# Kernel tuning notes

Hardware: AMD Instinct MI355X
Metric: run time of the kernel (lower is better)

Reference implementation:

```python
import math
import jax, jax.numpy as jnp
import numpy as np

# Matryoshka nested sizes (num_heads == 1, kv_groups == 1)
QK_SIZES = [512, 1024, 1536, 2048]
HEAD_SIZES = [512, 1024, 1536, 2048]
D_IN = 2048   # input_sizes[-1]
D_OUT = 2048  # output_sizes[-1]
NEG = -1e9


def setup_inputs() -> dict:
    key = jax.random.key(0)
    ks = jax.random.split(key, 5)
    B, S = 4, 2048
    x = jax.random.normal(ks[0], (B, S, D_IN), dtype=jnp.float32)
    mask = jnp.tril(jnp.ones((S, S), dtype=bool))  # causal boolean mask
    scale = 0.02
    Wq = jax.random.normal(ks[1], (D_IN, QK_SIZES[-1]), dtype=jnp.float32) * scale
    Wk = jax.random.normal(ks[2], (D_IN, QK_SIZES[-1]), dtype=jnp.float32) * scale
    Wv = jax.random.normal(ks[3], (D_IN, HEAD_SIZES[-1]), dtype=jnp.float32) * scale
    Wo = jax.random.normal(ks[4], (HEAD_SIZES[-1], D_OUT), dtype=jnp.float32) * scale
    return {"x": x, "mask": mask, "Wq": Wq, "Wk": Wk, "Wv": Wv, "Wo": Wo}


def reference(x, mask, Wq, Wk, Wv, Wo):
    # x: [B, S, D_IN]; num_heads == 1 so we keep heads implicit.
    q = x @ Wq  # [B, S, qk_last]
    k = x @ Wk  # [B, S, qk_last]
    v = x @ Wv  # [B, S, head_last]
    mask_add = jnp.where(mask, 0.0, NEG).astype(x.dtype)  # [S, S]

    outs = []
    cum = None  # cumulative QK^T across nested qk slices
    prev_qk = 0
    prev_h = 0
    for qk, h in zip(QK_SIZES, HEAD_SIZES):
        dp = jnp.einsum("bqd,bkd->bqk", q[..., prev_qk:qk], k[..., prev_qk:qk])
        cum = dp if cum is None else cum + dp  # [B, S, S]
        logits = cum * (1.0 / math.sqrt(qk)) + mask_add
        attn = jax.nn.softmax(logits, axis=-1)
        outs.append(jnp.einsum("bqk,bkd->bqd", attn, v[..., prev_h:h]))
        prev_qk, prev_h = qk, h
    o = jnp.concatenate(outs, axis=-1)  # [B, S, head_last]
    return o @ Wo  # [B, S, D_OUT]
```

## Files before the change

kernel.cpp:

```cpp
#include <hip/hip_runtime.h>


typedef __attribute__((ext_vector_type(8))) short bf16x8;
typedef __attribute__((ext_vector_type(4))) float f32x4;
typedef unsigned short u16;
typedef unsigned int u32;

__device__ __forceinline__ u16 f2bf(float f) {
  union { float f; u32 u; } v; v.f = f;
  u32 r = v.u + 0x7fffu + ((v.u >> 16) & 1u);
  return (u16)(r >> 16);
}
__device__ __forceinline__ float bf2f(u16 b) {
  union { u32 u; float f; } v; v.u = ((u32)b) << 16;
  return v.f;
}
struct alignas(16) U16x8 { u16 v[8]; };

#define GLDS(gp, lp)                                                      \
  __builtin_amdgcn_global_load_lds(                                       \
      (const __attribute__((address_space(1))) void*)(gp),                \
      (__attribute__((address_space(3))) void*)(lp), 16, 0, 0)


__global__ __launch_bounds__(256) void conv_f32_bf16(const float* __restrict__ in,
                                                     u16* __restrict__ out) {
  size_t i = ((size_t)blockIdx.x * 256 + threadIdx.x) * 8;
  float4 a = *(const float4*)(in + i);
  float4 b = *(const float4*)(in + i + 4);
  U16x8 w;
  w.v[0] = f2bf(a.x); w.v[1] = f2bf(a.y); w.v[2] = f2bf(a.z); w.v[3] = f2bf(a.w);
  w.v[4] = f2bf(b.x); w.v[5] = f2bf(b.y); w.v[6] = f2bf(b.z); w.v[7] = f2bf(b.w);
  *(U16x8*)(out + i) = w;
}

__global__ __launch_bounds__(256) void transpose_conv4(const float* __restrict__ W0,
                                                       const float* __restrict__ W1,
                                                       const float* __restrict__ W2,
                                                       const float* __restrict__ W3,
                                                       u16* __restrict__ out) {
  const int D = 2048;
  const float* in = (blockIdx.z == 0) ? W0 : (blockIdx.z == 1) ? W1
                  : (blockIdx.z == 2) ? W2 : W3;
  u16* o = out + (size_t)blockIdx.z * D * D;
  __shared__ float t[32][33];
  int bx = blockIdx.x * 32, by = blockIdx.y * 32;
  int tx = threadIdx.x & 31, ty = threadIdx.x >> 5;
#pragma unroll
  for (int i = 0; i < 32; i += 8)
    t[ty + i][tx] = in[(size_t)(by + ty + i) * D + bx + tx];
  __syncthreads();
#pragma unroll
  for (int i = 0; i < 32; i += 8)
    o[(size_t)(bx + ty + i) * D + by + tx] = f2bf(t[tx][ty + i]);
}

__global__ __launch_bounds__(256) void transpose_bf16(const u16* __restrict__ in,
                                                      u16* __restrict__ out) {
  const int D = 2048;
  size_t zoff = (size_t)blockIdx.z * D * D;
  in += zoff; out += zoff;
  __shared__ u16 t[32][34];
  int bx = blockIdx.x * 32, by = blockIdx.y * 32;
  int tx = threadIdx.x & 31, ty = threadIdx.x >> 5;
#pragma unroll
  for (int i = 0; i < 32; i += 8)
    t[ty + i][tx] = in[(size_t)(by + ty + i) * D + bx + tx];
  __syncthreads();
#pragma unroll
  for (int i = 0; i < 32; i += 8)
    out[(size_t)(bx + ty + i) * D + by + tx] = t[tx][ty + i];
}

template <bool OUT_BF16>
__global__ __launch_bounds__(512, 2) void gemmQKV(
    const u16* __restrict__ A, int lda,
    const u16* __restrict__ B, int ldb,
    void* __restrict__ Cv, int ldc,
    int K, int nmat, long long sBm, long long sCm) {
  extern __shared__ char smem[];
  u16* const As = (u16*)smem;
  u16* const Bs = (u16*)(smem + 65536);

  const u32 wg = blockIdx.x;
  const int n0 = (int)(wg & 7u) * 256;
  const u32 c = wg >> 3;
  const int mat = (int)(c % (u32)nmat);
  const int m0 = (int)(c / (u32)nmat) * 256;

  B += (size_t)mat * sBm;

  const int tid = threadIdx.x;
  const int lane = tid & 63, wave = tid >> 6;
  const int wm = (wave >> 2) * 128;
  const int wn = (wave & 3) * 64;
  const int fr = lane & 15, kgrp = lane >> 4;
  const u32 lo = (u32)(wave * 1024);

  const int srow = tid >> 2;
  const int ssl = (tid & 3) ^ ((srow >> 1) & 3);
  const u16* gA0 = A + (size_t)(m0 + srow) * lda + ssl * 8;
  const u16* gA1 = gA0 + (size_t)128 * lda;
  const u16* gB0 = B + (size_t)(n0 + srow) * ldb + ssl * 8;
  const u16* gB1 = gB0 + (size_t)128 * ldb;

  const int koe = (kgrp ^ ((fr >> 1) & 3)) * 8;

#define STG(slot, kOff) do {                                              \
    char* la = (char*)As + (slot) * 16384 + lo;                           \
    char* lb = (char*)Bs + (slot) * 16384 + lo;                           \
    GLDS(gA0 + (kOff), la);                                               \
    GLDS(gA1 + (kOff), la + 8192);                                        \
    GLDS(gB0 + (kOff), lb);                                               \
    GLDS(gB1 + (kOff), lb + 8192);                                        \
  } while (0)

#define READF(FA, FB, sl) do {                                            \
    const u16* as_ = As + (sl) * 8192;                                    \
    const u16* bs_ = Bs + (sl) * 8192;                                    \
    _Pragma("unroll") for (int n_ = 0; n_ < 4; ++n_)                      \
      FB[n_] = *(const bf16x8*)&bs_[((wn + n_ * 16 + fr) << 5) + koe];    \
    _Pragma("unroll") for (int m_ = 0; m_ < 8; ++m_)                      \
      FA[m_] = *(const bf16x8*)&as_[((wm + m_ * 16 + fr) << 5) + koe];    \
  } while (0)

#define MMCL(FA, FB) do {                                                 \
    __builtin_amdgcn_s_setprio(1);                                        \
    _Pragma("unroll") for (int m_ = 0; m_ < 8; ++m_)                      \
    _Pragma("unroll") for (int n_ = 0; n_ < 4; ++n_)                      \
      acc[m_][n_] = __builtin_amdgcn_mfma_f32_16x16x32_bf16(              \
          FA[m_], FB[n_], acc[m_][n_], 0, 0, 0);                          \
    __builtin_amdgcn_s_setprio(0);                                        \
  } while (0)

#define ITER(tt, CA, CB, NA, NB) do {                                     \
    if ((tt) + 3 < NT)                                                    \
      asm volatile("s_waitcnt lgkmcnt(12)" ::: "memory");                 \
    if ((tt) <= NT - 3)                                                   \
      asm volatile("s_waitcnt vmcnt(4)" ::: "memory");                    \
    else if ((tt) == NT - 2)                                              \
      asm volatile("s_waitcnt vmcnt(0)" ::: "memory");                    \
    if ((tt) <= NT - 2) {                                                 \
      __builtin_amdgcn_s_barrier();                                       \
      __builtin_amdgcn_sched_barrier(0);                                  \
    }                                                                     \
    if ((tt) + 3 < NT) STG(((tt) + 3) & 3, ((tt) + 3) * 32);              \
    if ((tt) + 1 < NT) READF(NA, NB, ((tt) + 1) & 3);                     \
    MMCL(CA, CB);                                                         \
  } while (0)

  f32x4 acc[8][4];
#pragma unroll
  for (int m = 0; m < 8; ++m)
#pragma unroll
    for (int n = 0; n < 4; ++n)
#pragma unroll
      for (int j = 0; j < 4; ++j) acc[m][n][j] = 0.f;

  const int NT = K >> 5;
  bf16x8 fA0[8], fB0[4], fA1[8], fB1[4];

  STG(0, 0);
  STG(1, 32);
  STG(2, 64);
  asm volatile("s_waitcnt vmcnt(8)" ::: "memory");
  __builtin_amdgcn_s_barrier();
  __builtin_amdgcn_sched_barrier(0);
  READF(fA0, fB0, 0);

  for (int tt = 0; tt < NT; tt += 2) {
    ITER(tt, fA0, fB0, fA1, fB1);
    ITER(tt + 1, fA1, fB1, fA0, fB0);
  }
#undef ITER
#undef MMCL
#undef READF
#undef STG

  const int cl = lane & 15, rb = (lane >> 4) * 4;
  if (OUT_BF16) {
    u16* C = (u16*)Cv + (size_t)mat * sCm;
#pragma unroll
    for (int m = 0; m < 8; ++m)
#pragma unroll
      for (int n = 0; n < 4; ++n)
#pragma unroll
        for (int j = 0; j < 4; ++j)
          C[(size_t)(m0 + wm + m * 16 + rb + j) * ldc + (n0 + wn + n * 16 + cl)] =
              f2bf(acc[m][n][j]);
  } else {
    float* C = (float*)Cv + (size_t)mat * sCm;
#pragma unroll
    for (int m = 0; m < 8; ++m)
#pragma unroll
      for (int n = 0; n < 4; ++n)
#pragma unroll
        for (int j = 0; j < 4; ++j)
          C[(size_t)(m0 + wm + m * 16 + rb + j) * ldc + (n0 + wn + n * 16 + cl)] =
              acc[m][n][j];
  }
}

template <bool OUT_BF16>
__global__ __launch_bounds__(256, 2) void gemm128(
    const u16* __restrict__ A, int lda,
    const u16* __restrict__ B, int ldb,
    void* __restrict__ Cv, int ldc,
    int K, int nmat, long long sBm, long long sCm) {
  constexpr int RPS = 64;
  extern __shared__ char smem[];
  u16* const As = (u16*)smem;
  u16* const Bs = (u16*)smem + 2 * 128 * 32;

  const u32 wg = blockIdx.x;
  const int n0 = (int)(wg & 7u) * 256;
  const u32 c = wg >> 3;
  const int mat = (int)(c % (u32)nmat);
  const int m0 = (int)(c / (u32)nmat) * 128;

  B += (size_t)mat * sBm;

  const int tid = threadIdx.x;
  const int lane = tid & 63, wave = tid >> 6;
  const int wn = (wave & 3) * 64;
  const int fr = lane & 15, kgrp = lane >> 4;
  const u32 lo = (u32)(wave * 1024);

  const int srow = tid >> 2;
  const int ssl = (tid & 3) ^ ((srow >> 1) & 3);
  const u16* gA = A + (size_t)(m0 + srow) * lda + ssl * 8;
  const u16* gB = B + (size_t)(n0 + srow) * ldb + ssl * 8;

  const int koe = (kgrp ^ ((fr >> 1) & 3)) * 8;

#define STG(slot, kOff) do {                                              \
    char* la = (char*)As + (slot) * 8192 + lo;                            \
    char* lb = (char*)Bs + (slot) * 16384 + lo;                           \
    _Pragma("unroll") for (int j_ = 0; j_ < 2; ++j_)                      \
      GLDS(gA + (size_t)j_ * RPS * lda + (kOff), la + j_ * RPS * 64);     \
    _Pragma("unroll") for (int j_ = 0; j_ < 4; ++j_)                      \
      GLDS(gB + (size_t)j_ * RPS * ldb + (kOff), lb + j_ * RPS * 64);     \
  } while (0)

#define READF(FA, FB, sl) do {                                            \
    const u16* as_ = As + (sl) * 4096;                                    \
    const u16* bs_ = Bs + (sl) * 8192;                                    \
    _Pragma("unroll") for (int n_ = 0; n_ < 4; ++n_)                      \
      FB[n_] = *(const bf16x8*)&bs_[((wn + n_ * 16 + fr) << 5) + koe];    \
    _Pragma("unroll") for (int m_ = 0; m_ < 8; ++m_)                      \
      FA[m_] = *(const bf16x8*)&as_[(((m_ * 16 + fr)) << 5) + koe];       \
  } while (0)

#define MMCL(FA, FB) do {                                                 \
    __builtin_amdgcn_s_setprio(1);                                        \
    _Pragma("unroll") for (int m_ = 0; m_ < 8; ++m_)                      \
    _Pragma("unroll") for (int n_ = 0; n_ < 4; ++n_)                      \
      acc[m_][n_] = __builtin_amdgcn_mfma_f32_16x16x32_bf16(              \
          FA[m_], FB[n_], acc[m_][n_], 0, 0, 0);                          \
    __builtin_amdgcn_s_setprio(0);                                        \
  } while (0)

#define ITER(tt, CA, CB, NA, NB) do {                                     \
    if ((tt) + 1 < NT) READF(NA, NB, ((tt) + 1) & 1);                     \
    if ((tt) + 2 < NT) {                                                  \
      asm volatile("s_waitcnt lgkmcnt(12)" ::: "memory");                 \
      __builtin_amdgcn_s_barrier();                                       \
      STG((tt) & 1, ((tt) + 2) * 32);                                     \
      __builtin_amdgcn_sched_barrier(0);                                  \
    }                                                                     \
    MMCL(CA, CB);                                                         \
    if ((tt) + 2 < NT) {                                                  \
      asm volatile("s_waitcnt vmcnt(0)" ::: "memory");                    \
      __builtin_amdgcn_s_barrier();                                       \
    }                                                                     \
  } while (0)

  f32x4 acc[8][4];
#pragma unroll
  for (int m = 0; m < 8; ++m)
#pragma unroll
    for (int n = 0; n < 4; ++n)
#pragma unroll
      for (int j = 0; j < 4; ++j) acc[m][n][j] = 0.f;

  const int NT = K >> 5;
  bf16x8 fA0[8], fB0[4], fA1[8], fB1[4];

  STG(0, 0);
  STG(1, 32);
  asm volatile("s_waitcnt vmcnt(0)" ::: "memory");
  __builtin_amdgcn_s_barrier();
  __builtin_amdgcn_sched_barrier(0);
  READF(fA0, fB0, 0);

  for (int tt = 0; tt < NT; tt += 2) {
    ITER(tt, fA0, fB0, fA1, fB1);
    ITER(tt + 1, fA1, fB1, fA0, fB0);
  }
#undef ITER
#undef MMCL
#undef READF
#undef STG

  const int cl = lane & 15, rb = (lane >> 4) * 4;
  if (OUT_BF16) {
    u16* C = (u16*)Cv + (size_t)mat * sCm;
#pragma unroll
    for (int m = 0; m < 8; ++m)
#pragma unroll
      for (int n = 0; n < 4; ++n)
#pragma unroll
        for (int j = 0; j < 4; ++j)
          C[(size_t)(m0 + m * 16 + rb + j) * ldc + (n0 + wn + n * 16 + cl)] =
              f2bf(acc[m][n][j]);
  } else {
    float* C = (float*)Cv + (size_t)mat * sCm;
#pragma unroll
    for (int m = 0; m < 8; ++m)
#pragma unroll
      for (int n = 0; n < 4; ++n)
#pragma unroll
        for (int j = 0; j < 4; ++j)
          C[(size_t)(m0 + m * 16 + rb + j) * ldc + (n0 + wn + n * 16 + cl)] =
              acc[m][n][j];
  }
}

__global__ __launch_bounds__(256) void qk_mega(
    const u16* __restrict__ A, const u16* __restrict__ B,
    u16* __restrict__ snapA, u16* __restrict__ snapB,
    float scaleA, float scaleB,
    const u16* __restrict__ initSrc, float initScale) {
  const int lda = 2048;
  const int m0 = blockIdx.y * 128, n0 = blockIdx.x * 128;
  if (n0 >= m0 + 128) return;
  const size_t zWE = (size_t)blockIdx.z * 4194304ull;
  extern __shared__ char smem[];
  u16* const As = (u16*)smem;
  u16* const Bs = (u16*)(smem + 32768);

  const int tid = threadIdx.x;
  const int lane = tid & 63, wave = tid >> 6;
  const int wm = (wave >> 1) * 64, wn = (wave & 1) * 64;
  const int fr = lane & 15;
  const int col = lane & 15, rb = (lane >> 4) * 4;
  const u32 lo = (u32)(wave * 1024);

  const int srow = tid >> 2;
  const int ssl = (tid & 3) ^ ((srow >> 1) & 3);
  const u16* gA0 = A + zWE + (size_t)(m0 + srow) * lda + ssl * 8;
  const u16* gA1 = gA0 + (size_t)64 * lda;
  const u16* gB0 = B + zWE + (size_t)(n0 + srow) * lda + ssl * 8;
  const u16* gB1 = gB0 + (size_t)64 * lda;

  const int koe = ((lane >> 4) ^ ((fr >> 1) & 3)) * 8;

#define QSTG(slot, kOff) do {                                             \
    char* la = (char*)As + (slot) * 8192 + lo;                            \
    char* lb = (char*)Bs + (slot) * 8192 + lo;                            \
    GLDS(gA0 + (kOff), la);                                               \
    GLDS(gA1 + (kOff), la + 4096);                                        \
    GLDS(gB0 + (kOff), lb);                                               \
    GLDS(gB1 + (kOff), lb + 4096);                                        \
  } while (0)

#define QREADF(FA, FB, sl) do {                                           \
    const u16* as_ = As + (sl) * 4096;                                    \
    const u16* bs_ = Bs + (sl) * 4096;                                    \
    _Pragma("unroll") for (int n_ = 0; n_ < 4; ++n_)                      \
      FB[n_] = *(const bf16x8*)&bs_[((wn + n_ * 16 + fr) << 5) + koe];    \
    _Pragma("unroll") for (int m_ = 0; m_ < 4; ++m_)                      \
      FA[m_] = *(const bf16x8*)&as_[((wm + m_ * 16 + fr) << 5) + koe];    \
  } while (0)

#define QMMCL(FA, FB) do {                                                \
    __builtin_amdgcn_s_setprio(1);                                        \
    _Pragma("unroll") for (int m_ = 0; m_ < 4; ++m_)                      \
    _Pragma("unroll") for (int n_ = 0; n_ < 4; ++n_)                      \
      acc[m_][n_] = __builtin_amdgcn_mfma_f32_16x16x32_bf16(              \
          FA[m_], FB[n_], acc[m_][n_], 0, 0, 0);                          \
    __builtin_amdgcn_s_setprio(0);                                        \
  } while (0)

#define QITER(tt, CA, CB, NA, NB) do {                                    \
    if ((tt) + 3 < 32)                                                    \
      asm volatile("s_waitcnt lgkmcnt(8)" ::: "memory");                  \
    if ((tt) <= 29)                                                       \
      asm volatile("s_waitcnt vmcnt(4)" ::: "memory");                    \
    else if ((tt) == 30)                                                  \
      asm volatile("s_waitcnt vmcnt(0)" ::: "memory");                    \
    if ((tt) <= 30) {                                                     \
      __builtin_amdgcn_s_barrier();                                       \
      __builtin_amdgcn_sched_barrier(0);                                  \
    }                                                                     \
    if ((tt) + 3 < 32) QSTG(((tt) + 3) & 3, ((tt) + 3) * 32);             \
    if ((tt) + 1 < 32) QREADF(NA, NB, ((tt) + 1) & 3);                    \
    QMMCL(CA, CB);                                                        \
  } while (0)

  f32x4 acc[4][4];
  if (initSrc) {
    const u16* ip = initSrc + zWE;
#pragma unroll
    for (int m = 0; m < 4; ++m)
#pragma unroll
      for (int n = 0; n < 4; ++n)
#pragma unroll
        for (int j = 0; j < 4; ++j)
          acc[m][n][j] = bf2f(ip[(size_t)(m0 + wm + m * 16 + rb + j) * 2048 +
                                 (n0 + wn + n * 16 + col)]) * initScale;
  } else {
#pragma unroll
    for (int m = 0; m < 4; ++m)
#pragma unroll
      for (int n = 0; n < 4; ++n)
#pragma unroll
        for (int j = 0; j < 4; ++j) acc[m][n][j] = 0.f;
  }

#define SNAPW(ptr, scl)                                                                \
  do {                                                                                 \
    u16* sp = (ptr) + zWE;                                                             \
    _Pragma("unroll") for (int m = 0; m < 4; ++m)                                      \
    _Pragma("unroll") for (int n = 0; n < 4; ++n)                                      \
    _Pragma("unroll") for (int j = 0; j < 4; ++j)                                      \
        sp[(size_t)(m0 + wm + m * 16 + rb + j) * 2048 + (n0 + wn + n * 16 + col)] =    \
            f2bf(acc[m][n][j] * (scl));                                                \
  } while (0)

  bf16x8 fA0[4], fB0[4], fA1[4], fB1[4];
  QSTG(0, 0);
  QSTG(1, 32);
  QSTG(2, 64);
  asm volatile("s_waitcnt vmcnt(8)" ::: "memory");
  __builtin_amdgcn_s_barrier();
  __builtin_amdgcn_sched_barrier(0);
  QREADF(fA0, fB0, 0);

  for (int tt = 0; tt < 32; tt += 2) {
    QITER(tt, fA0, fB0, fA1, fB1);
    QITER(tt + 1, fA1, fB1, fA0, fB0);
    if (tt == 14) SNAPW(snapA, scaleA);
  }
  SNAPW(snapB, scaleB);
#undef QITER
#undef QMMCL
#undef QREADF
#undef QSTG
#undef SNAPW
}

__global__ __launch_bounds__(256) void gemm_pv(
    const u16* __restrict__ A0, const u16* __restrict__ A1,
    const u16* __restrict__ vT, u16* __restrict__ o, int s0) {
  const int z = blockIdx.z;
  const int half = z >> 2, b = z & 3, s = s0 + half;
  const u16* A = (half ? A1 : A0) + (size_t)b * 4194304ull;
  const u16* B = vT + (size_t)b * 4194304ull + (size_t)s * 512 * 2048;
  u16* C = o + (size_t)b * 4194304ull + s * 512;

  const int n0 = blockIdx.x * 128, m0 = blockIdx.y * 128;
  const int NT = (m0 + 128) >> 5;
  extern __shared__ char smem[];
  u16* const As = (u16*)smem;
  u16* const Bs = (u16*)(smem + 32768);

  const int tid = threadIdx.x;
  const int lane = tid & 63, wave = tid >> 6;
  const int wm = (wave >> 1) * 64, wn = (wave & 1) * 64;
  const int fr = lane & 15;
  const u32 lo = (u32)(wave * 1024);

  const int srow = tid >> 2;
  const int ssl = (tid & 3) ^ ((srow >> 1) & 3);
  const u16* gA0 = A + (size_t)(m0 + srow) * 2048 + ssl * 8;
  const u16* gA1 = gA0 + (size_t)64 * 2048;
  const u16* gB0 = B + (size_t)(n0 + srow) * 2048 + ssl * 8;
  const u16* gB1 = gB0 + (size_t)64 * 2048;

  const int koe = ((lane >> 4) ^ ((fr >> 1) & 3)) * 8;

#define PSTG(slot, kOff) do {                                             \
    char* la = (char*)As + (slot) * 8192 + lo;                            \
    char* lb = (char*)Bs + (slot) * 8192 + lo;                            \
    GLDS(gA0 + (kOff), la);                                               \
    GLDS(gA1 + (kOff), la + 4096);                                        \
    GLDS(gB0 + (kOff), lb);                                               \
    GLDS(gB1 + (kOff), lb + 4096);                                        \
  } while (0)

#define PREADF(FA, FB, sl) do {                                           \
    const u16* as_ = As + (sl) * 4096;                                    \
    const u16* bs_ = Bs + (sl) * 4096;                                    \
    _Pragma("unroll") for (int n_ = 0; n_ < 4; ++n_)                      \
      FB[n_] = *(const bf16x8*)&bs_[((wn + n_ * 16 + fr) << 5) + koe];    \
    _Pragma("unroll") for (int m_ = 0; m_ < 4; ++m_)                      \
      FA[m_] = *(const bf16x8*)&as_[((wm + m_ * 16 + fr) << 5) + koe];    \
  } while (0)

#define PMMCL(FA, FB) do {                                                \
    __builtin_amdgcn_s_setprio(1);                                        \
    _Pragma("unroll") for (int m_ = 0; m_ < 4; ++m_)                      \
    _Pragma("unroll") for (int n_ = 0; n_ < 4; ++n_)                      \
      acc[m_][n_] = __builtin_amdgcn_mfma_f32_16x16x32_bf16(              \
          FA[m_], FB[n_], acc[m_][n_], 0, 0, 0);                          \
    __builtin_amdgcn_s_setprio(0);                                        \
  } while (0)

#define PITER(tt, CA, CB, NA, NB) do {                                    \
    if ((tt) + 3 < NT)                                                    \
      asm volatile("s_waitcnt lgkmcnt(8)" ::: "memory");                  \
    if ((tt) <= NT - 3)                                                   \
      asm volatile("s_waitcnt vmcnt(4)" ::: "memory");                    \
    else if ((tt) == NT - 2)                                              \
      asm volatile("s_waitcnt vmcnt(0)" ::: "memory");                    \
    if ((tt) <= NT - 2) {                                                 \
      __builtin_amdgcn_s_barrier();                                       \
      __builtin_amdgcn_sched_barrier(0);                                  \
    }                                                                     \
    if ((tt) + 3 < NT) PSTG(((tt) + 3) & 3, ((tt) + 3) * 32);             \
    if ((tt) + 1 < NT) PREADF(NA, NB, ((tt) + 1) & 3);                    \
    PMMCL(CA, CB);                                                        \
  } while (0)

  f32x4 acc[4][4];
#pragma unroll
  for (int m = 0; m < 4; ++m)
#pragma unroll
    for (int n = 0; n < 4; ++n)
#pragma unroll
      for (int j = 0; j < 4; ++j) acc[m][n][j] = 0.f;

  bf16x8 fA0[4], fB0[4], fA1[4], fB1[4];
  PSTG(0, 0);
  PSTG(1, 32);
  PSTG(2, 64);
  asm volatile("s_waitcnt vmcnt(8)" ::: "memory");
  __builtin_amdgcn_s_barrier();
  __builtin_amdgcn_sched_barrier(0);
  PREADF(fA0, fB0, 0);

  for (int tt = 0; tt < NT; tt += 2) {
    PITER(tt, fA0, fB0, fA1, fB1);
    PITER(tt + 1, fA1, fB1, fA0, fB0);
  }
#undef PITER
#undef PMMCL
#undef PREADF
#undef PSTG

  const int col = lane & 15, rb = (lane >> 4) * 4;
#pragma unroll
  for (int m = 0; m < 4; ++m)
#pragma unroll
    for (int n = 0; n < 4; ++n)
#pragma unroll
      for (int j = 0; j < 4; ++j)
        C[(size_t)(m0 + wm + m * 16 + rb + j) * 2048 + (n0 + wn + n * 16 + col)] =
            f2bf(acc[m][n][j]);
}

__global__ __launch_bounds__(256) void softmax_dual(const u16* __restrict__ in0,
                                                    u16* __restrict__ out0,
                                                    const u16* __restrict__ in1,
                                                    u16* __restrict__ out1) {
  const int S = 2048;
  const int y = blockIdx.y;
  const u16* in  = (y < 4) ? in0  : in1;
  u16* out       = (y < 4) ? out0 : out1;
  const size_t WEz = (size_t)S * S * (y & 3);
  const int r = blockIdx.x;
  const int tid = threadIdx.x;
  const int lane = tid & 63, wave = tid >> 6;
  const int c0 = tid * 8;
  const int nvalid = r + 1;
  const int nwrite = (r & ~127) + 128;
  const u16* rowp = in + WEz + (size_t)r * S;

  float x[8];
  if (c0 < nvalid) {
    U16x8 a = *(const U16x8*)(rowp + c0);
#pragma unroll
    for (int i = 0; i < 8; ++i) x[i] = bf2f(a.v[i]);
  } else {
#pragma unroll
    for (int i = 0; i < 8; ++i) x[i] = 0.f;
  }

  float mx = -3e38f;
#pragma unroll
  for (int i = 0; i < 8; ++i)
    if (c0 + i < nvalid) mx = fmaxf(mx, x[i]);
#pragma unroll
  for (int off = 32; off > 0; off >>= 1) mx = fmaxf(mx, __shfl_xor(mx, off));
  __shared__ float redm[4], reds[4];
  if (lane == 0) redm[wave] = mx;
  __syncthreads();
  mx = fmaxf(fmaxf(redm[0], redm[1]), fmaxf(redm[2], redm[3]));

  float e[8], sum = 0.f;
#pragma unroll
  for (int i = 0; i < 8; ++i) {
    e[i] = (c0 + i < nvalid) ? __expf(x[i] - mx) : 0.f;
    sum += e[i];
  }
#pragma unroll
  for (int off = 32; off > 0; off >>= 1) sum += __shfl_xor(sum, off);
  if (lane == 0) reds[wave] = sum;
  __syncthreads();
  sum = reds[0] + reds[1] + reds[2] + reds[3];
  float inv = 1.f / sum;

  if (c0 < nwrite) {
    U16x8 w;
#pragma unroll
    for (int i = 0; i < 8; ++i) w.v[i] = f2bf(e[i] * inv);
    *(U16x8*)(out + WEz + (size_t)r * S + c0) = w;
  }
}

extern "C" void kernel_launch(void* const* d_in, const int* in_sizes, int n_in,
                              void* d_out, int out_size, void* d_ws, size_t ws_size,
                              hipStream_t stream) {
  (void)in_sizes; (void)n_in; (void)out_size; (void)ws_size;
  const float* x  = (const float*)d_in[0];
  const float* Wq = (const float*)d_in[2];
  const float* Wk = (const float*)d_in[3];
  const float* Wv = (const float*)d_in[4];
  const float* Wo = (const float*)d_in[5];
  float* out = (float*)d_out;

  char* w = (char*)d_ws;
  const size_t R  = 33554432ull;
  const long long WE = 4194304LL;

  u16* xb  = (u16*)(w);
  u16* wT  = (u16*)(w + R);
  u16* wqT = wT;
  u16* woT = wT + 3 * WE;
  u16* q   = (u16*)(w + 2 * R);
  u16* kk  = (u16*)(w + 3 * R);
  u16* v   = (u16*)(w + 4 * R);
  u16* vT  = (u16*)(w + 5 * R);
  u16* o   = v;
  u16* attnx = xb;
  u16* slot0 = (u16*)d_out;
  u16* slot1 = slot0 + 16777216ull;

  const float sc0 = 1.0f / sqrtf(512.0f);
  const float sc1 = 1.0f / sqrtf(1024.0f);
  const float sc2 = 1.0f / sqrtf(1536.0f);
  const float sc3 = 1.0f / sqrtf(2048.0f);

  hipFuncSetAttribute(reinterpret_cast<const void*>(&gemmQKV<true>),
                      hipFuncAttributeMaxDynamicSharedMemorySize, 131072);
  hipFuncSetAttribute(reinterpret_cast<const void*>(&gemm128<false>),
                      hipFuncAttributeMaxDynamicSharedMemorySize, 49152);
  hipFuncSetAttribute(reinterpret_cast<const void*>(&qk_mega),
                      hipFuncAttributeMaxDynamicSharedMemorySize, 65536);
  hipFuncSetAttribute(reinterpret_cast<const void*>(&gemm_pv),
                      hipFuncAttributeMaxDynamicSharedMemorySize, 65536);

  conv_f32_bf16<<<8192, 256, 0, stream>>>(x, xb);
  transpose_conv4<<<dim3(64, 64, 4), 256, 0, stream>>>(Wq, Wk, Wv, Wo, wT);
  gemmQKV<true><<<dim3(768), 512, 131072, stream>>>(
      xb, 2048, wqT, 2048, q, 2048, 2048, 3, WE, 16777216LL);
  transpose_bf16<<<dim3(64, 64, 4), 256, 0, stream>>>(v, vT);
  qk_mega<<<dim3(16, 16, 4), 256, 65536, stream>>>(q, kk, slot0, slot1, sc0, sc1,
                                                   nullptr, 0.f);
  softmax_dual<<<dim3(2048, 8), 256, 0, stream>>>(slot0, slot0, slot1, attnx);
  gemm_pv<<<dim3(4, 16, 8), 256, 65536, stream>>>(slot0, attnx, vT, o, 0);
  qk_mega<<<dim3(16, 16, 4), 256, 65536, stream>>>(q + 1024, kk + 1024, slot0,
                                                   slot1, sc2, sc3, slot1, 32.0f);
  softmax_dual<<<dim3(2048, 8), 256, 0, stream>>>(slot0, slot0, slot1, slot1);
  gemm_pv<<<dim3(4, 16, 8), 256, 65536, stream>>>(slot0, slot1, vT, o, 2);
  gemm128<false><<<dim3(512), 256, 49152, stream>>>(
      o, 2048, woT, 2048, out, 2048, 2048, 1, 0LL, 0LL);
}
```

Baseline: 529.6 us.

## Rewrite projection GEMM as eight-phase pipelined kernel and reuse it for output projection

Replaces the QKV GEMM main loop with an eight-phase schedule per 128-wide K chunk. Each phase loads half the A fragments and issues one half-tile global-to-LDS load, then runs a smaller MFMA cluster between barriers, with a changed LDS swizzle. The separate 128-row output-projection GEMM is removed and the same 256x256 kernel is used for it, launching 256 workgroups of 512 threads instead of 512 of 256. K is hardcoded to 2048, and the extra barriers plus fewer output-projection workgroups may reduce occupancy or overlap.

```diff
diff --git a/kernel.cpp b/kernel.cpp
--- a/kernel.cpp
+++ b/kernel.cpp
@@ -73,21 +73,19 @@
 }
 
 template <bool OUT_BF16>
-__global__ __launch_bounds__(512, 2) void gemmQKV(
+__global__ __launch_bounds__(512, 2) void gemm8p(
     const u16* __restrict__ A, int lda,
     const u16* __restrict__ B, int ldb,
     void* __restrict__ Cv, int ldc,
-    int K, int nmat, long long sBm, long long sCm) {
+    int nmat, long long sBm, long long sCm) {
   extern __shared__ char smem[];
-  u16* const As = (u16*)smem;
-  u16* const Bs = (u16*)(smem + 65536);
+  u16* const S = (u16*)smem;
 
   const u32 wg = blockIdx.x;
   const int n0 = (int)(wg & 7u) * 256;
   const u32 c = wg >> 3;
   const int mat = (int)(c % (u32)nmat);
   const int m0 = (int)(c / (u32)nmat) * 256;
-
   B += (size_t)mat * sBm;
 
   const int tid = threadIdx.x;
@@ -98,55 +96,45 @@
   const u32 lo = (u32)(wave * 1024);
 
   const int srow = tid >> 2;
-  const int ssl = (tid & 3) ^ ((srow >> 1) & 3);
-  const u16* gA0 = A + (size_t)(m0 + srow) * lda + ssl * 8;
-  const u16* gA1 = gA0 + (size_t)128 * lda;
-  const u16* gB0 = B + (size_t)(n0 + srow) * ldb + ssl * 8;
-  const u16* gB1 = gB0 + (size_t)128 * ldb;
-
-  const int koe = (kgrp ^ ((fr >> 1) & 3)) * 8;
-
-#define STG(slot, kOff) do {                                              \
-    char* la = (char*)As + (slot) * 16384 + lo;                           \
-    char* lb = (char*)Bs + (slot) * 16384 + lo;                           \
-    GLDS(gA0 + (kOff), la);                                               \
-    GLDS(gA1 + (kOff), la + 8192);                                        \
-    GLDS(gB0 + (kOff), lb);                                               \
-    GLDS(gB1 + (kOff), lb + 8192);                                        \
-  } while (0)
-
-#define READF(FA, FB, sl) do {                                            \
-    const u16* as_ = As + (sl) * 8192;                                    \
-    const u16* bs_ = Bs + (sl) * 8192;                                    \
-    _Pragma("unroll") for (int n_ = 0; n_ < 4; ++n_)                      \
-      FB[n_] = *(const bf16x8*)&bs_[((wn + n_ * 16 + fr) << 5) + koe];    \
-    _Pragma("unroll") for (int m_ = 0; m_ < 8; ++m_)                      \
-      FA[m_] = *(const bf16x8*)&as_[((wm + m_ * 16 + fr) << 5) + koe];    \
-  } while (0)
-
-#define MMCL(FA, FB) do {                                                 \
-    __builtin_amdgcn_s_setprio(1);                                        \
-    _Pragma("unroll") for (int m_ = 0; m_ < 8; ++m_)                      \
-    _Pragma("unroll") for (int n_ = 0; n_ < 4; ++n_)                      \
-      acc[m_][n_] = __builtin_amdgcn_mfma_f32_16x16x32_bf16(              \
-          FA[m_], FB[n_], acc[m_][n_], 0, 0, 0);                          \
-    __builtin_amdgcn_s_setprio(0);                                        \
-  } while (0)
-
-#define ITER(tt, CA, CB, NA, NB) do {                                     \
-    if ((tt) + 3 < NT)                                                    \
-      asm volatile("s_waitcnt lgkmcnt(12)" ::: "memory");                 \
-    if ((tt) <= NT - 3)                                                   \
-      asm volatile("s_waitcnt vmcnt(4)" ::: "memory");                    \
-    else if ((tt) == NT - 2)                                              \
-      asm volatile("s_waitcnt vmcnt(0)" ::: "memory");                    \
-    if ((tt) <= NT - 2) {                                                 \
-      __builtin_amdgcn_s_barrier();                                       \
-      __builtin_amdgcn_sched_barrier(0);                                  \
-    }                                                                     \
-    if ((tt) + 3 < NT) STG(((tt) + 3) & 3, ((tt) + 3) * 32);              \
-    if ((tt) + 1 < NT) READF(NA, NB, ((tt) + 1) & 3);                     \
-    MMCL(CA, CB);                                                         \
+  const int g = (tid & 3) ^ (srow & 3);
+  const u16* gA = A + (size_t)(m0 + srow) * lda + g * 8;
+  const u16* gB = B + (size_t)(n0 + srow) * ldb + g * 8;
+
+  const int rbase = (kgrp ^ (fr & 3)) * 8;
+  const int aoff = (wm + fr) * 32 + rbase;
+  const int boff = 32768 + (wn + fr) * 32 + rbase;
+
+#define STG8(ISB, slot, koff) do {                                       \
+    char* d_ = (char*)smem + ((ISB) ? 65536 : 0) + (slot) * 16384 + lo;  \
+    const u16* gp_ = (ISB) ? gB : gA;                                    \
+    const int ld_ = (ISB) ? ldb : lda;                                   \
+    GLDS(gp_ + (koff), d_);                                              \
+    GLDS(gp_ + (size_t)128 * ld_ + (koff), d_ + 8192);                   \
+  } while (0)
+
+#define PH8(LP, kb, DOSTG, WC) do {                                      \
+    constexpr int sl_ = (LP) >> 1;                                       \
+    constexpr int mh_ = (LP) & 1;                                        \
+    if (mh_ == 0) {                                                      \
+      _Pragma("unroll") for (int n_ = 0; n_ < 4; ++n_)                   \
+        fB[n_] = *(const bf16x8*)&S[boff + sl_ * 8192 + n_ * 512];       \
+    }                                                                    \
+    _Pragma("unroll") for (int a_ = 0; a_ < 4; ++a_)                     \
+      fA[a_] = *(const bf16x8*)&S[aoff + sl_ * 8192 + mh_ * 2048 + a_ * 512]; \
+    if (DOSTG) STG8(mh_, (3 + sl_) & 3, (kb) + (3 + sl_) * 32);          \
+    if ((WC) == 4) asm volatile("s_waitcnt vmcnt(4)" ::: "memory");      \
+    else if ((WC) == 0) asm volatile("s_waitcnt vmcnt(0)" ::: "memory"); \
+    __builtin_amdgcn_s_barrier();                                        \
+    asm volatile("s_waitcnt lgkmcnt(0)" ::: "memory");                   \
+    __builtin_amdgcn_sched_barrier(0);                                   \
+    __builtin_amdgcn_s_setprio(1);                                       \
+    _Pragma("unroll") for (int a_ = 0; a_ < 4; ++a_)                     \
+      _Pragma("unroll") for (int n_ = 0; n_ < 4; ++n_)                   \
+        acc[mh_ * 4 + a_][n_] = __builtin_amdgcn_mfma_f32_16x16x32_bf16( \
+            fA[a_], fB[n_], acc[mh_ * 4 + a_][n_], 0, 0, 0);             \
+    __builtin_amdgcn_s_setprio(0);                                       \
+    __builtin_amdgcn_s_barrier();                                        \
+    __builtin_amdgcn_sched_barrier(0);                                   \
   } while (0)
 
   f32x4 acc[8][4];
@@ -157,25 +145,31 @@
 #pragma unroll
       for (int j = 0; j < 4; ++j) acc[m][n][j] = 0.f;
 
-  const int NT = K >> 5;
-  bf16x8 fA0[8], fB0[4], fA1[8], fB1[4];
-
-  STG(0, 0);
-  STG(1, 32);
-  STG(2, 64);
+  bf16x8 fA[4], fB[4];
+
+  STG8(0, 0, 0);   STG8(1, 0, 0);
+  STG8(0, 1, 32);  STG8(1, 1, 32);
+  STG8(0, 2, 64);  STG8(1, 2, 64);
   asm volatile("s_waitcnt vmcnt(8)" ::: "memory");
   __builtin_amdgcn_s_barrier();
   __builtin_amdgcn_sched_barrier(0);
-  READF(fA0, fB0, 0);
-
-  for (int tt = 0; tt < NT; tt += 2) {
-    ITER(tt, fA0, fB0, fA1, fB1);
-    ITER(tt + 1, fA1, fB1, fA0, fB0);
-  }
-#undef ITER
-#undef MMCL
-#undef READF
-#undef STG
+
+  for (int i = 0; i < 15; ++i) {
+    const int kb = i * 128;
+    PH8(0, kb, 1, -1);  PH8(1, kb, 1, 4);
+    PH8(2, kb, 1, -1);  PH8(3, kb, 1, 4);
+    PH8(4, kb, 1, -1);  PH8(5, kb, 1, 4);
+    PH8(6, kb, 1, -1);  PH8(7, kb, 1, 4);
+  }
+  {
+    const int kb = 15 * 128;
+    PH8(0, kb, 1, -1);  PH8(1, kb, 1, 4);
+    PH8(2, kb, 0, -1);  PH8(3, kb, 0, -1);
+    PH8(4, kb, 0, -1);  PH8(5, kb, 0, 0);
+    PH8(6, kb, 0, -1);  PH8(7, kb, 0, -1);
+  }
+#undef PH8
+#undef STG8
 
   const int cl = lane & 15, rb = (lane >> 4) * 4;
   if (OUT_BF16) {
@@ -197,131 +191,6 @@
 #pragma unroll
         for (int j = 0; j < 4; ++j)
           C[(size_t)(m0 + wm + m * 16 + rb + j) * ldc + (n0 + wn + n * 16 + cl)] =
-              acc[m][n][j];
-  }
-}
-
-template <bool OUT_BF16>
-__global__ __launch_bounds__(256, 2) void gemm128(
-    const u16* __restrict__ A, int lda,
-    const u16* __restrict__ B, int ldb,
-    void* __restrict__ Cv, int ldc,
-    int K, int nmat, long long sBm, long long sCm) {
-  constexpr int RPS = 64;
-  extern __shared__ char smem[];
-  u16* const As = (u16*)smem;
-  u16* const Bs = (u16*)smem + 2 * 128 * 32;
-
-  const u32 wg = blockIdx.x;
-  const int n0 = (int)(wg & 7u) * 256;
-  const u32 c = wg >> 3;
-  const int mat = (int)(c % (u32)nmat);
-  const int m0 = (int)(c / (u32)nmat) * 128;
-
-  B += (size_t)mat * sBm;
-
-  const int tid = threadIdx.x;
-  const int lane = tid & 63, wave = tid >> 6;
-  const int wn = (wave & 3) * 64;
-  const int fr = lane & 15, kgrp = lane >> 4;
-  const u32 lo = (u32)(wave * 1024);
-
-  const int srow = tid >> 2;
-  const int ssl = (tid & 3) ^ ((srow >> 1) & 3);
-  const u16* gA = A + (size_t)(m0 + srow) * lda + ssl * 8;
-  const u16* gB = B + (size_t)(n0 + srow) * ldb + ssl * 8;
-
-  const int koe = (kgrp ^ ((fr >> 1) & 3)) * 8;
-
-#define STG(slot, kOff) do {                                              \
-    char* la = (char*)As + (slot) * 8192 + lo;                            \
-    char* lb = (char*)Bs + (slot) * 16384 + lo;                           \
-    _Pragma("unroll") for (int j_ = 0; j_ < 2; ++j_)                      \
-      GLDS(gA + (size_t)j_ * RPS * lda + (kOff), la + j_ * RPS * 64);     \
-    _Pragma("unroll") for (int j_ = 0; j_ < 4; ++j_)                      \
-      GLDS(gB + (size_t)j_ * RPS * ldb + (kOff), lb + j_ * RPS * 64);     \
-  } while (0)
-
-#define READF(FA, FB, sl) do {                                            \
-    const u16* as_ = As + (sl) * 4096;                                    \
-    const u16* bs_ = Bs + (sl) * 8192;                                    \
-    _Pragma("unroll") for (int n_ = 0; n_ < 4; ++n_)                      \
-      FB[n_] = *(const bf16x8*)&bs_[((wn + n_ * 16 + fr) << 5) + koe];    \
-    _Pragma("unroll") for (int m_ = 0; m_ < 8; ++m_)                      \
-      FA[m_] = *(const bf16x8*)&as_[(((m_ * 16 + fr)) << 5) + koe];       \
-  } while (0)
-
-#define MMCL(FA, FB) do {                                                 \
-    __builtin_amdgcn_s_setprio(1);                                        \
-    _Pragma("unroll") for (int m_ = 0; m_ < 8; ++m_)                      \
-    _Pragma("unroll") for (int n_ = 0; n_ < 4; ++n_)                      \
-      acc[m_][n_] = __builtin_amdgcn_mfma_f32_16x16x32_bf16(              \
-          FA[m_], FB[n_], acc[m_][n_], 0, 0, 0);                          \
-    __builtin_amdgcn_s_setprio(0);                                        \
-  } while (0)
-
-#define ITER(tt, CA, CB, NA, NB) do {                                     \
-    if ((tt) + 1 < NT) READF(NA, NB, ((tt) + 1) & 1);                     \
-    if ((tt) + 2 < NT) {                                                  \
-      asm volatile("s_waitcnt lgkmcnt(12)" ::: "memory");                 \
-      __builtin_amdgcn_s_barrier();                                       \
-      STG((tt) & 1, ((tt) + 2) * 32);                                     \
-      __builtin_amdgcn_sched_barrier(0);                                  \
-    }                                                                     \
-    MMCL(CA, CB);                                                         \
-    if ((tt) + 2 < NT) {                                                  \
-      asm volatile("s_waitcnt vmcnt(0)" ::: "memory");                    \
-      __builtin_amdgcn_s_barrier();                                       \
-    }                                                                     \
-  } while (0)
-
-  f32x4 acc[8][4];
-#pragma unroll
-  for (int m = 0; m < 8; ++m)
-#pragma unroll
-    for (int n = 0; n < 4; ++n)
-#pragma unroll
-      for (int j = 0; j < 4; ++j) acc[m][n][j] = 0.f;
-
-  const int NT = K >> 5;
-  bf16x8 fA0[8], fB0[4], fA1[8], fB1[4];
-
-  STG(0, 0);
-  STG(1, 32);
-  asm volatile("s_waitcnt vmcnt(0)" ::: "memory");
-  __builtin_amdgcn_s_barrier();
-  __builtin_amdgcn_sched_barrier(0);
-  READF(fA0, fB0, 0);
-
-  for (int tt = 0; tt < NT; tt += 2) {
-    ITER(tt, fA0, fB0, fA1, fB1);
-    ITER(tt + 1, fA1, fB1, fA0, fB0);
-  }
-#undef ITER
-#undef MMCL
-#undef READF
-#undef STG
-
-  const int cl = lane & 15, rb = (lane >> 4) * 4;
-  if (OUT_BF16) {
-    u16* C = (u16*)Cv + (size_t)mat * sCm;
-#pragma unroll
-    for (int m = 0; m < 8; ++m)
-#pragma unroll
-      for (int n = 0; n < 4; ++n)
-#pragma unroll
-        for (int j = 0; j < 4; ++j)
-          C[(size_t)(m0 + m * 16 + rb + j) * ldc + (n0 + wn + n * 16 + cl)] =
-              f2bf(acc[m][n][j]);
-  } else {
-    float* C = (float*)Cv + (size_t)mat * sCm;
-#pragma unroll
-    for (int m = 0; m < 8; ++m)
-#pragma unroll
-      for (int n = 0; n < 4; ++n)
-#pragma unroll
-        for (int j = 0; j < 4; ++j)
-          C[(size_t)(m0 + m * 16 + rb + j) * ldc + (n0 + wn + n * 16 + cl)] =
               acc[m][n][j];
   }
 }
@@ -652,10 +521,10 @@
   const float sc2 = 1.0f / sqrtf(1536.0f);
   const float sc3 = 1.0f / sqrtf(2048.0f);
 
-  hipFuncSetAttribute(reinterpret_cast<const void*>(&gemmQKV<true>),
+  hipFuncSetAttribute(reinterpret_cast<const void*>(&gemm8p<true>),
                       hipFuncAttributeMaxDynamicSharedMemorySize, 131072);
-  hipFuncSetAttribute(reinterpret_cast<const void*>(&gemm128<false>),
-                      hipFuncAttributeMaxDynamicSharedMemorySize, 49152);
+  hipFuncSetAttribute(reinterpret_cast<const void*>(&gemm8p<false>),
+                      hipFuncAttributeMaxDynamicSharedMemorySize, 131072);
   hipFuncSetAttribute(reinterpret_cast<const void*>(&qk_mega),
                       hipFuncAttributeMaxDynamicSharedMemorySize, 65536);
   hipFuncSetAttribute(reinterpret_cast<const void*>(&gemm_pv),
@@ -663,8 +532,8 @@
 
   conv_f32_bf16<<<8192, 256, 0, stream>>>(x, xb);
   transpose_conv4<<<dim3(64, 64, 4), 256, 0, stream>>>(Wq, Wk, Wv, Wo, wT);
-  gemmQKV<true><<<dim3(768), 512, 131072, stream>>>(
-      xb, 2048, wqT, 2048, q, 2048, 2048, 3, WE, 16777216LL);
+  gemm8p<true><<<dim3(768), 512, 131072, stream>>>(
+      xb, 2048, wqT, 2048, q, 2048, 3, WE, 16777216LL);
   transpose_bf16<<<dim3(64, 64, 4), 256, 0, stream>>>(v, vT);
   qk_mega<<<dim3(16, 16, 4), 256, 65536, stream>>>(q, kk, slot0, slot1, sc0, sc1,
                                                    nullptr, 0.f);
@@ -674,6 +543,6 @@
                                                    slot1, sc2, sc3, slot1, 32.0f);
   softmax_dual<<<dim3(2048, 8), 256, 0, stream>>>(slot0, slot0, slot1, slot1);
   gemm_pv<<<dim3(4, 16, 8), 256, 65536, stream>>>(slot0, slot1, vT, o, 2);
-  gemm128<false><<<dim3(512), 256, 49152, stream>>>(
-      o, 2048, woT, 2048, out, 2048, 2048, 1, 0LL, 0LL);
-}
+  gemm8p<false><<<dim3(256), 512, 131072, stream>>>(
+      o, 2048, woT, 2048, out, 2048, 1, 0LL, 0LL);
+}
```

Measured after the change: 526.2 us. No clear change (-0.6%).
